# Kernel tuning notes

Hardware: AMD Instinct MI355X
Metric: run time of the kernel (lower is better)

Reference implementation:

```python
import jax, jax.numpy as jnp
import numpy as np

EMB = 1024
HEADS = 16
HEAD_DIM = EMB // HEADS
EPS = 1e-5


def setup_inputs() -> dict:
    key = jax.random.key(0)
    ks = jax.random.split(key, 10)
    B, T, D = 2, 2048, EMB
    s = 1.0 / np.sqrt(D)
    inp = {
        "x": jax.random.normal(ks[0], (B, T, D), dtype=jnp.float32),
        "wq": jax.random.normal(ks[1], (D, D), dtype=jnp.float32) * s,
        "bq": jnp.zeros((D,), jnp.float32),
        "wk": jax.random.normal(ks[2], (D, D), dtype=jnp.float32) * s,
        "bk": jnp.zeros((D,), jnp.float32),
        "wv": jax.random.normal(ks[3], (D, D), dtype=jnp.float32) * s,
        "bv": jnp.zeros((D,), jnp.float32),
        "wo": jax.random.normal(ks[4], (D, D), dtype=jnp.float32) * s,
        "bo": jnp.zeros((D,), jnp.float32),
        "gamma": jnp.ones((D,), jnp.float32),
        "beta": jnp.zeros((D,), jnp.float32),
    }
    return inp


def _attention(x, wq, bq, wk, bk, wv, bv, wo, bo, gamma, beta):
    B, T, D = x.shape
    H, Hd = HEADS, HEAD_DIM
    q = (x @ wq + bq).reshape(B, T, H, Hd)
    k = (x @ wk + bk).reshape(B, T, H, Hd)
    v = (x @ wv + bv).reshape(B, T, H, Hd)
    # scores: [B, H, T, T]
    scores = jnp.einsum("bthd,bshd->bhts", q, k) / np.sqrt(Hd)
    attn = jax.nn.softmax(scores, axis=-1)  # dropout is identity in eval
    ctx = jnp.einsum("bhts,bshd->bthd", attn, v).reshape(B, T, D)
    out = ctx @ wo + bo
    y = x + out  # residual (dropout identity)
    mu = jnp.mean(y, axis=-1, keepdims=True)
    var = jnp.var(y, axis=-1, keepdims=True)
    return (y - mu) * jax.lax.rsqrt(var + EPS) * gamma + beta


def reference(x, wq, bq, wk, bk, wv, bv, wo, bo, gamma, beta):
    return _attention(x, wq, bq, wk, bk, wv, bv, wo, bo, gamma, beta)
```

## Files before the change

### kernel.cpp

```cpp
#include <hip/hip_runtime.h>

#define BSZ   2
#define TSEQ  2048
#define DMOD  1024
#define NHEAD 16
#define HDIM  64
#define MROW  (BSZ*TSEQ)
#define LNEPS 1e-5f
#define QSCALE 0.18033688011f

typedef __bf16 bf16x8 __attribute__((ext_vector_type(8)));
typedef float  f32x4  __attribute__((ext_vector_type(4)));
typedef unsigned short us8 __attribute__((ext_vector_type(8)));
typedef unsigned short us4 __attribute__((ext_vector_type(4)));

__device__ __forceinline__ unsigned short f2bf(float f) {
    unsigned u = __float_as_uint(f);
    u += 0x7FFF + ((u >> 16) & 1);
    return (unsigned short)(u >> 16);
}
__device__ __forceinline__ float bf2f(unsigned short u) {
    return __uint_as_float((unsigned)u << 16);
}

__device__ __forceinline__ float fexp2(float x) {
#if __has_builtin(__builtin_amdgcn_exp2f)
    return __builtin_amdgcn_exp2f(x);
#else
    return __expf(x * 0.6931471805599453f);
#endif
}

__device__ __forceinline__ void gld_lds16(const void* g, void* l) {
    __builtin_amdgcn_global_load_lds(
        (const __attribute__((address_space(1))) unsigned int*)g,
        (__attribute__((address_space(3))) unsigned int*)l, 16, 0, 0);
}

__global__ __launch_bounds__(256) void prep_k(
    const float* __restrict__ x,
    const float* __restrict__ wq, const float* __restrict__ wk,
    const float* __restrict__ wv, const float* __restrict__ wo,
    unsigned short* __restrict__ Xb,
    unsigned short* __restrict__ WqkvT, unsigned short* __restrict__ WoT)
{
    const int tid = threadIdx.x;
    if (blockIdx.x < 2048) {
        const size_t i = ((size_t)blockIdx.x * 256 + tid) * 8;
        float4 a = *(const float4*)&x[i];
        float4 b = *(const float4*)&x[i + 4];
        union { unsigned short u[8]; uint4 v; } o;
        o.u[0]=f2bf(a.x); o.u[1]=f2bf(a.y); o.u[2]=f2bf(a.z); o.u[3]=f2bf(a.w);
        o.u[4]=f2bf(b.x); o.u[5]=f2bf(b.y); o.u[6]=f2bf(b.z); o.u[7]=f2bf(b.w);
        *(uint4*)&Xb[i] = o.v;
        return;
    }
    __shared__ float T[64][68];
    const int id = blockIdx.x - 2048;
    const int z  = id >> 8;
    const int bx = id & 15;
    const int by = (id >> 4) & 15;
    const float* W = (z == 0) ? wq : (z == 1) ? wk : (z == 2) ? wv : wo;
    unsigned short* Wt = (z < 3) ? (WqkvT + (size_t)z*1024*1024) : WoT;
    const int lr = tid >> 4, lc = (tid & 15) * 4;
    #pragma unroll
    for (int p = 0; p < 4; ++p) {
        const int kk = p*16 + lr;
        float4 v = *(const float4*)&W[(size_t)(by*64 + kk)*1024 + bx*64 + lc];
        T[lc+0][kk] = v.x; T[lc+1][kk] = v.y; T[lc+2][kk] = v.z; T[lc+3][kk] = v.w;
    }
    __syncthreads();
    #pragma unroll
    for (int p = 0; p < 2; ++p) {
        const int nl = p*32 + (tid >> 3);
        const int kb = (tid & 7) * 8;
        float4 a = *(const float4*)&T[nl][kb];
        float4 b = *(const float4*)&T[nl][kb+4];
        union { unsigned short u[8]; uint4 v; } o;
        o.u[0]=f2bf(a.x); o.u[1]=f2bf(a.y); o.u[2]=f2bf(a.z); o.u[3]=f2bf(a.w);
        o.u[4]=f2bf(b.x); o.u[5]=f2bf(b.y); o.u[6]=f2bf(b.z); o.u[7]=f2bf(b.w);
        *(uint4*)&Wt[(size_t)(bx*64 + nl)*1024 + by*64 + kb] = o.v;
    }
}


#define PH_SYNC() do { __builtin_amdgcn_s_barrier(); \
    asm volatile("s_waitcnt lgkmcnt(0)" ::: "memory"); \
    __builtin_amdgcn_sched_barrier(0); } while (0)

template<int N>
__device__ __forceinline__ void vmwait() {
    if constexpr (N == 0)      asm volatile("s_waitcnt vmcnt(0)" ::: "memory");
    else if constexpr (N == 3) asm volatile("s_waitcnt vmcnt(3)" ::: "memory");
    else                       asm volatile("s_waitcnt vmcnt(4)" ::: "memory");
}

template<int NB>
struct CoreT {
    const unsigned short *sA, *sB;
    unsigned short *A0w, *A1w, *B0w, *B1w;
    const unsigned short *fA0, *fA1, *fB0, *fB1;
    int swz0, swz1;
};

__device__ __forceinline__ void stageA4(const unsigned short* s, unsigned short* d) {
    #pragma unroll
    for (int u = 0; u < 4; ++u) gld_lds16(s + u*64*1024, d + u*4096);
}
template<int NB>
__device__ __forceinline__ void stageBall(const unsigned short* s, unsigned short* d) {
    #pragma unroll
    for (int u = 0; u < NB; ++u) gld_lds16(s + u*64*1024, d + u*4096);
}
__device__ __forceinline__ void stageB01(const unsigned short* s, unsigned short* d) {
    gld_lds16(s, d); gld_lds16(s + 64*1024, d + 4096);
}
template<int NB>
__device__ __forceinline__ void stageBrest(const unsigned short* s, unsigned short* d) {
    #pragma unroll
    for (int u = 2; u < NB; ++u) gld_lds16(s + u*64*1024, d + u*4096);
}

template<int NB>
__device__ __forceinline__ void core_setup(CoreT<NB>& C, unsigned short* LDS,
    const unsigned short* A, const unsigned short* Bt, int bm, int bn, int kbase)
{
    const int tid = threadIdx.x;
    const int w = tid >> 6, lane = tid & 63;
    const int quad = lane >> 4, l16 = lane & 15;
    const int wm = w >> 2, wn = w & 3;
    const int r_l = lane >> 3, c_l = lane & 7;
    C.sA = A  + (size_t)(bm + w*8 + r_l)*1024 + (c_l ^ r_l)*8 + kbase;
    C.sB = Bt + (size_t)(bn + w*8 + r_l)*1024 + (c_l ^ r_l)*8 + kbase;
    unsigned short* A0 = LDS;
    unsigned short* A1 = LDS + 16384;
    unsigned short* B0 = LDS + 32768;
    unsigned short* B1 = B0 + NB*4096;
    C.A0w = A0 + w*512; C.A1w = A1 + w*512;
    C.B0w = B0 + w*512; C.B1w = B1 + w*512;
    C.fA0 = A0 + (wm*128 + l16)*64; C.fA1 = A1 + (wm*128 + l16)*64;
    C.fB0 = B0 + (wn*NB*16 + l16)*64;  C.fB1 = B1 + (wn*NB*16 + l16)*64;
    C.swz0 = ( quad      ^ (l16 & 7)) * 8;
    C.swz1 = ((4 + quad) ^ (l16 & 7)) * 8;
}

template<int NB>
__device__ __forceinline__ void ld_b(const CoreT<NB>& C, bf16x8 (&bfr)[NB][2],
                                     const unsigned short* fB) {
    #pragma unroll
    for (int n = 0; n < NB; ++n) {
        bfr[n][0] = *(const bf16x8*)(fB + n*1024 + C.swz0);
        bfr[n][1] = *(const bf16x8*)(fB + n*1024 + C.swz1);
    }
}

template<int Q, int NB>
__device__ __forceinline__ void ld_a(const CoreT<NB>& C, bf16x8 (&af)[2][2],
                                     const unsigned short* fA) {
    #pragma unroll
    for (int dm = 0; dm < 2; ++dm) {
        af[dm][0] = *(const bf16x8*)(fA + (Q*2+dm)*1024 + C.swz0);
        af[dm][1] = *(const bf16x8*)(fA + (Q*2+dm)*1024 + C.swz1);
    }
}

template<int Q, int NB>
__device__ __forceinline__ void mma_q(f32x4 (&acc)[8][NB], bf16x8 (&af)[2][2],
                                      bf16x8 (&bfr)[NB][2]) {
    __builtin_amdgcn_s_setprio(1);
    #pragma unroll
    for (int dm = 0; dm < 2; ++dm)
        #pragma unroll
        for (int n = 0; n < NB; ++n) {
            f32x4 t = acc[Q*2+dm][n];
            t = __builtin_amdgcn_mfma_f32_16x16x32_bf16(af[dm][0], bfr[n][0], t, 0, 0, 0);
            t = __builtin_amdgcn_mfma_f32_16x16x32_bf16(af[dm][1], bfr[n][1], t, 0, 0, 0);
            acc[Q*2+dm][n] = t;
        }
    __builtin_amdgcn_s_setprio(0);
}

template<int NIT, int NB>
__device__ __forceinline__ void core_kloop(const CoreT<NB>& C, f32x4 (&acc)[8][NB])
{
    stageA4(C.sA, C.A0w);
    stageBall<NB>(C.sB,      C.B0w);
    stageBall<NB>(C.sB + 64, C.B1w);
    vmwait<NB>();
    __builtin_amdgcn_s_barrier();

    bf16x8 bfr[NB][2];
    bf16x8 af[2][2];

    #pragma unroll 1
    for (int it = 0; it < NIT - 1; ++it) {
        const int kk = it * 128;
        ld_b<NB>(C, bfr, C.fB0);
        ld_a<0,NB>(C, af, C.fA0);
        stageA4(C.sA + kk + 64, C.A1w);
        PH_SYNC();  mma_q<0,NB>(acc, af, bfr);
        __builtin_amdgcn_s_barrier();
        ld_a<1,NB>(C, af, C.fA0);
        stageB01(C.sB + kk + 128, C.B0w);
        PH_SYNC();  mma_q<1,NB>(acc, af, bfr);
        __builtin_amdgcn_s_barrier();
        ld_a<2,NB>(C, af, C.fA0);
        stageBrest<NB>(C.sB + kk + 128, C.B0w);
        PH_SYNC();  mma_q<2,NB>(acc, af, bfr);
        __builtin_amdgcn_s_barrier();
        ld_a<3,NB>(C, af, C.fA0);
        PH_SYNC();  mma_q<3,NB>(acc, af, bfr);
        vmwait<NB>();
        __builtin_amdgcn_s_barrier();
        ld_b<NB>(C, bfr, C.fB1);
        ld_a<0,NB>(C, af, C.fA1);
        stageA4(C.sA + kk + 128, C.A0w);
        PH_SYNC();  mma_q<0,NB>(acc, af, bfr);
        __builtin_amdgcn_s_barrier();
        ld_a<1,NB>(C, af, C.fA1);
        stageB01(C.sB + kk + 192, C.B1w);
        PH_SYNC();  mma_q<1,NB>(acc, af, bfr);
        __builtin_amdgcn_s_barrier();
        ld_a<2,NB>(C, af, C.fA1);
        stageBrest<NB>(C.sB + kk + 192, C.B1w);
        PH_SYNC();  mma_q<2,NB>(acc, af, bfr);
        __builtin_amdgcn_s_barrier();
        ld_a<3,NB>(C, af, C.fA1);
        PH_SYNC();  mma_q<3,NB>(acc, af, bfr);
        vmwait<NB>();
        __builtin_amdgcn_s_barrier();
    }

    {
        const int kk = (NIT - 1) * 128;
        ld_b<NB>(C, bfr, C.fB0);
        ld_a<0,NB>(C, af, C.fA0);
        stageA4(C.sA + kk + 64, C.A1w);
        PH_SYNC();  mma_q<0,NB>(acc, af, bfr);
        __builtin_amdgcn_s_barrier();
        ld_a<1,NB>(C, af, C.fA0); PH_SYNC(); mma_q<1,NB>(acc, af, bfr); __builtin_amdgcn_s_barrier();
        ld_a<2,NB>(C, af, C.fA0); PH_SYNC(); mma_q<2,NB>(acc, af, bfr); __builtin_amdgcn_s_barrier();
        ld_a<3,NB>(C, af, C.fA0); PH_SYNC(); mma_q<3,NB>(acc, af, bfr);
        vmwait<0>();
        __builtin_amdgcn_s_barrier();
        ld_b<NB>(C, bfr, C.fB1);
        ld_a<0,NB>(C, af, C.fA1); PH_SYNC(); mma_q<0,NB>(acc, af, bfr); __builtin_amdgcn_s_barrier();
        ld_a<1,NB>(C, af, C.fA1); PH_SYNC(); mma_q<1,NB>(acc, af, bfr); __builtin_amdgcn_s_barrier();
        ld_a<2,NB>(C, af, C.fA1); PH_SYNC(); mma_q<2,NB>(acc, af, bfr); __builtin_amdgcn_s_barrier();
        ld_a<3,NB>(C, af, C.fA1); PH_SYNC(); mma_q<3,NB>(acc, af, bfr);
    }
}

__global__ __launch_bounds__(512, 1) void gemm_qkv_k(
    const unsigned short* __restrict__ A, const unsigned short* __restrict__ Bt,
    const float* __restrict__ b0, const float* __restrict__ b1,
    const float* __restrict__ b2,
    unsigned short* __restrict__ oQ, unsigned short* __restrict__ oK,
    unsigned short* __restrict__ oV)
{
    extern __shared__ unsigned short LDS[];
    const int ob = blockIdx.x;
    const int wg = (ob & 7) * 32 + (ob >> 3);
    const int by = wg >> 4, bx = wg & 15;
    const int bm = by * 256, bn = bx * 192;

    CoreT<3> C;
    core_setup<3>(C, LDS, A, Bt, bm, bn, 0);

    f32x4 acc[8][3];
    #pragma unroll
    for (int i = 0; i < 8; ++i)
        #pragma unroll
        for (int j = 0; j < 3; ++j) acc[i][j] = (f32x4){0.f,0.f,0.f,0.f};

    core_kloop<8,3>(C, acc);

    const int tid = threadIdx.x;
    const int w = tid >> 6, lane = tid & 63;
    const int quad = lane >> 4, l16 = lane & 15;
    const int wm = w >> 2, wn = w & 3;
    #pragma unroll
    for (int n = 0; n < 3; ++n) {
        const int c0  = bn + wn*48 + n*16;
        const int seg = c0 >> 10;
        const int cl0 = c0 & 1023;
        if (seg < 2) {
            unsigned short* O = (seg == 0) ? oQ : oK;
            const float sc = (seg == 0) ? QSCALE : 1.0f;
            const float* bias = (seg == 0) ? b0 : b1;
            const int col = cl0 + l16;
            const float bs = bias[col];
            #pragma unroll
            for (int m = 0; m < 8; ++m)
                #pragma unroll
                for (int r = 0; r < 4; ++r) {
                    const int grow = bm + wm*128 + m*16 + quad*4 + r;
                    O[(size_t)grow*1024 + col] = f2bf((acc[m][n][r] + bs) * sc);
                }
        } else {
            const int ch = cl0 + l16;
            const float bs = b2[ch];
            #pragma unroll
            for (int m = 0; m < 8; ++m) {
                const int grow0 = bm + wm*128 + m*16 + quad*4;
                us4 o;
                #pragma unroll
                for (int r = 0; r < 4; ++r) o[r] = f2bf(acc[m][n][r] + bs);
                *(us4*)&oV[(size_t)ch*MROW + grow0] = o;
            }
        }
    }
}

__global__ __launch_bounds__(512, 2) void gemm_proj_k(
    const unsigned short* __restrict__ A, const unsigned short* __restrict__ Bt,
    unsigned short* __restrict__ P)
{
    extern __shared__ unsigned short LDS[];
    const int ob = blockIdx.x;
    const int wg = (ob & 7) * 8 + (ob >> 3);
    const int by = wg >> 2, bx = wg & 3;
    const int kz = blockIdx.y;
    const int bm = by * 256, bn = bx * 256;

    CoreT<4> C;
    core_setup<4>(C, LDS, A, Bt, bm, bn, kz * 256);

    f32x4 acc[8][4];
    #pragma unroll
    for (int i = 0; i < 8; ++i)
        #pragma unroll
        for (int j = 0; j < 4; ++j) acc[i][j] = (f32x4){0.f,0.f,0.f,0.f};

    core_kloop<2,4>(C, acc);

    const int tid = threadIdx.x;
    const int w = tid >> 6, lane = tid & 63;
    const int quad = lane >> 4, l16 = lane & 15;
    const int wm = w >> 2, wn = w & 3;
    unsigned short* O = P + (size_t)kz*MROW*1024;
    #pragma unroll
    for (int n = 0; n < 4; ++n) {
        const int col = bn + wn*64 + n*16 + l16;
        #pragma unroll
        for (int m = 0; m < 8; ++m)
            #pragma unroll
            for (int r = 0; r < 4; ++r) {
                const int grow = bm + wm*128 + m*16 + quad*4 + r;
                O[(size_t)grow*1024 + col] = f2bf(acc[m][n][r]);
            }
    }
}

__global__ __launch_bounds__(256, 2) void attn_k(
    const unsigned short* __restrict__ Qg,
    const unsigned short* __restrict__ Kg,
    const unsigned short* __restrict__ Vtg,
    unsigned short* __restrict__ CTX)
{
    extern __shared__ __align__(16) char lds_raw[];
    unsigned short* KV = (unsigned short*)lds_raw;
    unsigned short* Qs = (unsigned short*)lds_raw;
    float* Od = (float*)lds_raw;
    float* Ld = (float*)(lds_raw + 65536);

    const int tid  = threadIdx.x;
    const int wv   = tid >> 6;
    const int lane = tid & 63;
    const int quad = lane >> 4;
    const int l16  = lane & 15;
    const int wq   = wv & 1;
    const int wk   = wv >> 1;
    const int qb   = blockIdx.x * 128;
    const int h    = blockIdx.y;
    const int b    = blockIdx.z;

    {
        const int row = tid & 127, cb = (tid >> 7) * 32;
        const unsigned short* Qrow = Qg + ((size_t)(b*TSEQ + qb + row))*DMOD + h*HDIM + cb;
        #pragma unroll
        for (int j = 0; j < 4; ++j)
            *(us8*)&Qs[row*72 + cb + j*8] = *(const us8*)&Qrow[j*8];
    }
    __syncthreads();
    bf16x8 qf[4][2];
    #pragma unroll
    for (int nt = 0; nt < 4; ++nt)
        #pragma unroll
        for (int kh = 0; kh < 2; ++kh)
            qf[nt][kh] = *(const bf16x8*)&Qs[(wq*64 + nt*16 + l16)*72 + kh*32 + quad*8];
    __syncthreads();

    const int sr = lane >> 3;
    const int sc = lane & 7;
    const bool isK = (wv < 2);
    const int half = wv & 1;
    const unsigned short* gbase;
    unsigned int goff[8];
    unsigned short* ldstb;
    if (isK) {
        gbase = Kg + ((size_t)(b*TSEQ + half*1024))*DMOD + h*HDIM;
        #pragma unroll
        for (int s = 0; s < 8; ++s) {
            const int R = s*8 + sr;
            const int gc = sc ^ ((R ^ (R >> 2)) & 7);
            goff[s] = (unsigned)(R*DMOD + gc*8);
        }
        ldstb = KV + half*4096;
    } else {
        gbase = Vtg + ((size_t)(h*HDIM))*MROW + b*TSEQ + half*1024;
        #pragma unroll
        for (int s = 0; s < 8; ++s) {
            const int D = s*8 + sr;
            const int gc = sc ^ (D & 7);
            goff[s] = (unsigned)(D*MROW + gc*8);
        }
        ldstb = KV + 16384 + half*4096;
    }
    const size_t gstep = isK ? (size_t)64*DMOD : (size_t)64;

    const int rowA_l = (l16 >> 2)*8 + (l16 & 3);
    const int rowB_l = rowA_l + 4;
    const int swA = (rowA_l ^ (rowA_l >> 2)) & 7;
    const int swB = (rowB_l ^ (rowB_l >> 2)) & 7;

    bf16x8 onef;
    { union { unsigned short u[8]; bf16x8 v; } o1;
      #pragma unroll
      for (int i = 0; i < 8; ++i) o1.u[i] = 0x3F80;
      onef = o1.v; }

    f32x4 oacc[4][4];
    f32x4 lacc[4];
    #pragma unroll
    for (int dt = 0; dt < 4; ++dt)
        #pragma unroll
        for (int nt = 0; nt < 4; ++nt) oacc[dt][nt] = (f32x4){0.f,0.f,0.f,0.f};
    #pragma unroll
    for (int nt = 0; nt < 4; ++nt) lacc[nt] = (f32x4){0.f,0.f,0.f,0.f};

    #pragma unroll
    for (int s = 0; s < 8; ++s)
        gld_lds16(gbase + goff[s], ldstb + s*512);
    __syncthreads();

    for (int it = 0; it < 16; ++it) {
        const int cbuf = (it & 1) * 8192;
        if (it < 15) {
            const unsigned short* gn = gbase + (size_t)(it+1)*gstep;
            unsigned short* d = ldstb + (cbuf ^ 8192);
            #pragma unroll
            for (int s = 0; s < 8; ++s)
                gld_lds16(gn + goff[s], d + s*512);
        }
        __builtin_amdgcn_sched_barrier(0);
        const unsigned short* KsW = KV + cbuf + wk*4096;
        const unsigned short* VsW = KV + 16384 + cbuf + wk*4096;

        #pragma unroll
        for (int gl = 0; gl < 2; ++gl) {
            const int rA = gl*32 + rowA_l;
            const int rB = gl*32 + rowB_l;
            bf16x8 ka0 = *(const bf16x8*)&KsW[rA*64 + ((quad     ^ swA))*8];
            bf16x8 ka1 = *(const bf16x8*)&KsW[rA*64 + (((4+quad) ^ swA))*8];
            bf16x8 kb0 = *(const bf16x8*)&KsW[rB*64 + ((quad     ^ swB))*8];
            bf16x8 kb1 = *(const bf16x8*)&KsW[rB*64 + (((4+quad) ^ swB))*8];
            bf16x8 vf[4];
            #pragma unroll
            for (int dt = 0; dt < 4; ++dt)
                vf[dt] = *(const bf16x8*)&VsW[(dt*16 + l16)*64 + ((gl*4 + quad) ^ (l16 & 7))*8];

            f32x4 sA[4], sB[4];
            #pragma unroll
            for (int nt = 0; nt < 4; ++nt) {
                f32x4 z = (f32x4){0.f,0.f,0.f,0.f};
                z = __builtin_amdgcn_mfma_f32_16x16x32_bf16(ka0, qf[nt][0], z, 0, 0, 0);
                sA[nt] = __builtin_amdgcn_mfma_f32_16x16x32_bf16(ka1, qf[nt][1], z, 0, 0, 0);
                f32x4 z2 = (f32x4){0.f,0.f,0.f,0.f};
                z2 = __builtin_amdgcn_mfma_f32_16x16x32_bf16(kb0, qf[nt][0], z2, 0, 0, 0);
                sB[nt] = __builtin_amdgcn_mfma_f32_16x16x32_bf16(kb1, qf[nt][1], z2, 0, 0, 0);
            }
            bf16x8 pf[4];
            #pragma unroll
            for (int nt = 0; nt < 4; ++nt) {
                float eA[4], eB[4];
                #pragma unroll
                for (int r = 0; r < 4; ++r) { eA[r] = fexp2(sA[nt][r]); eB[r] = fexp2(sB[nt][r]); }
                union { unsigned d[4]; bf16x8 v; } up;
                up.d[0] = __builtin_amdgcn_perm(__float_as_uint(eA[1]), __float_as_uint(eA[0]), 0x07060302);
                up.d[1] = __builtin_amdgcn_perm(__float_as_uint(eA[3]), __float_as_uint(eA[2]), 0x07060302);
                up.d[2] = __builtin_amdgcn_perm(__float_as_uint(eB[1]), __float_as_uint(eB[0]), 0x07060302);
                up.d[3] = __builtin_amdgcn_perm(__float_as_uint(eB[3]), __float_as_uint(eB[2]), 0x07060302);
                pf[nt] = up.v;
            }
            __builtin_amdgcn_s_setprio(1);
            #pragma unroll
            for (int nt = 0; nt < 4; ++nt) {
                lacc[nt] = __builtin_amdgcn_mfma_f32_16x16x32_bf16(onef, pf[nt], lacc[nt], 0, 0, 0);
                #pragma unroll
                for (int dt = 0; dt < 4; ++dt)
                    oacc[dt][nt] = __builtin_amdgcn_mfma_f32_16x16x32_bf16(vf[dt], pf[nt], oacc[dt][nt], 0, 0, 0);
            }
            __builtin_amdgcn_s_setprio(0);
        }
        __syncthreads();
    }

    if (wk == 0) {
        float* od = Od + wq*64*68;
        #pragma unroll
        for (int nt = 0; nt < 4; ++nt) {
            #pragma unroll
            for (int dt = 0; dt < 4; ++dt)
                *(f32x4*)&od[(nt*16 + l16)*68 + dt*16 + quad*4] = oacc[dt][nt];
            if (quad == 0) Ld[wq*64 + nt*16 + l16] = lacc[nt][0];
        }
    }
    __syncthreads();
    if (wk == 1) {
        const float* od = Od + wq*64*68;
        #pragma unroll
        for (int nt = 0; nt < 4; ++nt) {
            const float l = Ld[wq*64 + nt*16 + l16] + lacc[nt][0];
            const float inv = 1.f / l;
            const int q = qb + wq*64 + nt*16 + l16;
            unsigned short* crow = CTX + ((size_t)(b*TSEQ + q))*DMOD + h*HDIM;
            #pragma unroll
            for (int dt = 0; dt < 4; ++dt) {
                f32x4 p = *(const f32x4*)&od[(nt*16 + l16)*68 + dt*16 + quad*4];
                us4 o;
                #pragma unroll
                for (int r = 0; r < 4; ++r) o[r] = f2bf((p[r] + oacc[dt][nt][r]) * inv);
                *(us4*)&crow[dt*16 + quad*4] = o;
            }
        }
    }
}

__global__ __launch_bounds__(256) void red_ln_k(
    const float* __restrict__ x, const unsigned short* __restrict__ P,
    const float* __restrict__ bo,
    const float* __restrict__ gamma, const float* __restrict__ beta,
    float* __restrict__ out)
{
    __shared__ float rs[4], rss[4];
    const int row = blockIdx.x;
    const int tid = threadIdx.x;
    const int c = tid * 4;
    const float4 xv = *(const float4*)&x[(size_t)row*DMOD + c];
    const us4 p0 = *(const us4*)&P[(size_t)row*DMOD + c];
    const us4 p1 = *(const us4*)&P[(size_t)(MROW + row)*DMOD + c];
    const us4 p2 = *(const us4*)&P[(size_t)(2*MROW + row)*DMOD + c];
    const us4 p3 = *(const us4*)&P[(size_t)(3*MROW + row)*DMOD + c];
    const float4 bv4 = *(const float4*)&bo[c];
    const float v0 = xv.x + bf2f(p0[0]) + bf2f(p1[0]) + bf2f(p2[0]) + bf2f(p3[0]) + bv4.x;
    const float v1 = xv.y + bf2f(p0[1]) + bf2f(p1[1]) + bf2f(p2[1]) + bf2f(p3[1]) + bv4.y;
    const float v2 = xv.z + bf2f(p0[2]) + bf2f(p1[2]) + bf2f(p2[2]) + bf2f(p3[2]) + bv4.z;
    const float v3 = xv.w + bf2f(p0[3]) + bf2f(p1[3]) + bf2f(p2[3]) + bf2f(p3[3]) + bv4.w;
    float s  = v0 + v1 + v2 + v3;
    float ss = v0*v0 + v1*v1 + v2*v2 + v3*v3;
    #pragma unroll
    for (int o = 32; o > 0; o >>= 1) {
        s  += __shfl_down(s,  o, 64);
        ss += __shfl_down(ss, o, 64);
    }
    if ((tid & 63) == 0) { rs[tid >> 6] = s; rss[tid >> 6] = ss; }
    __syncthreads();
    s  = rs[0] + rs[1] + rs[2] + rs[3];
    ss = rss[0] + rss[1] + rss[2] + rss[3];
    const float mean = s * (1.f/DMOD);
    const float var  = ss * (1.f/DMOD) - mean*mean;
    const float rstd = rsqrtf(var + LNEPS);
    const float4 gv = *(const float4*)&gamma[c];
    const float4 bv = *(const float4*)&beta[c];
    float4 o;
    o.x = (v0 - mean)*rstd*gv.x + bv.x;
    o.y = (v1 - mean)*rstd*gv.y + bv.y;
    o.z = (v2 - mean)*rstd*gv.z + bv.z;
    o.w = (v3 - mean)*rstd*gv.w + bv.w;
    *(float4*)&out[(size_t)row*DMOD + c] = o;
}

extern "C" void kernel_launch(void* const* d_in, const int* in_sizes, int n_in,
                              void* d_out, int out_size, void* d_ws, size_t ws_size,
                              hipStream_t stream) {
    const float* x     = (const float*)d_in[0];
    const float* wq    = (const float*)d_in[1];
    const float* bq    = (const float*)d_in[2];
    const float* wk    = (const float*)d_in[3];
    const float* bk    = (const float*)d_in[4];
    const float* wvp   = (const float*)d_in[5];
    const float* bvp   = (const float*)d_in[6];
    const float* wo    = (const float*)d_in[7];
    const float* bo    = (const float*)d_in[8];
    const float* gamma = (const float*)d_in[9];
    const float* beta  = (const float*)d_in[10];
    float* out = (float*)d_out;

    unsigned short* Xb    = (unsigned short*)d_ws;
    unsigned short* WqkvT = Xb    + (size_t)MROW*DMOD;
    unsigned short* WoT   = WqkvT + (size_t)3072*1024;
    unsigned short* Qb    = WoT   + (size_t)1024*1024;
    unsigned short* Kb    = Qb    + (size_t)MROW*DMOD;
    unsigned short* VtG   = Kb    + (size_t)MROW*DMOD;
    unsigned short* CTXb  = VtG   + (size_t)DMOD*MROW;
    unsigned short* Pp    = CTXb  + (size_t)MROW*DMOD;

    prep_k<<<3072, 256, 0, stream>>>(x, wq, wk, wvp, wo, Xb, WqkvT, WoT);

    gemm_qkv_k<<<dim3(256), 512, 114688, stream>>>(
        Xb, WqkvT, bq, bk, bvp, Qb, Kb, VtG);

    attn_k<<<dim3(TSEQ/128, NHEAD, BSZ), 256, 66048, stream>>>(Qb, Kb, VtG, CTXb);

    gemm_proj_k<<<dim3(64, 4), 512, 131072, stream>>>(CTXb, WoT, Pp);

    red_ln_k<<<MROW, 256, 0, stream>>>(x, Pp, bo, gamma, beta, out);
}
```

Measured before the change: 193.7 us.

## Retile QKV, projection and attention kernels for different grid shapes and occupancy

The QKV GEMM moves from 256x192 tiles over 256 blocks to 256x256 tiles over 192 blocks, so each tile sits entirely within one Q/K/V segment. The projection GEMM uses 256x128 tiles with a 2-way split-K instead of 4-way, which halves the partial-sum traffic the LayerNorm reduction reads. Attention switches to 64-query blocks with a small single-buffered K/V LDS tile, a flattened swizzled grid over head and batch, and launch bounds of 4 blocks per CU, trading software double-buffering for higher occupancy. The attention loop now synchronises twice per iteration with no prefetch overlap, so load latency may be exposed.

```diff
diff --git a/kernel.cpp b/kernel.cpp
--- a/kernel.cpp
+++ b/kernel.cpp
@@ -91,6 +91,7 @@
 template<int N>
 __device__ __forceinline__ void vmwait() {
     if constexpr (N == 0)      asm volatile("s_waitcnt vmcnt(0)" ::: "memory");
+    else if constexpr (N == 2) asm volatile("s_waitcnt vmcnt(2)" ::: "memory");
     else if constexpr (N == 3) asm volatile("s_waitcnt vmcnt(3)" ::: "memory");
     else                       asm volatile("s_waitcnt vmcnt(4)" ::: "memory");
 }
@@ -260,35 +261,34 @@
 {
     extern __shared__ unsigned short LDS[];
     const int ob = blockIdx.x;
-    const int wg = (ob & 7) * 32 + (ob >> 3);
-    const int by = wg >> 4, bx = wg & 15;
-    const int bm = by * 256, bn = bx * 192;
-
-    CoreT<3> C;
-    core_setup<3>(C, LDS, A, Bt, bm, bn, 0);
-
-    f32x4 acc[8][3];
+    const int wg = (ob & 7) * 24 + (ob >> 3);
+    const int by = wg / 12, bx = wg - by*12;
+    const int bm = by * 256, bn = bx * 256;
+
+    CoreT<4> C;
+    core_setup<4>(C, LDS, A, Bt, bm, bn, 0);
+
+    f32x4 acc[8][4];
     #pragma unroll
     for (int i = 0; i < 8; ++i)
         #pragma unroll
-        for (int j = 0; j < 3; ++j) acc[i][j] = (f32x4){0.f,0.f,0.f,0.f};
-
-    core_kloop<8,3>(C, acc);
+        for (int j = 0; j < 4; ++j) acc[i][j] = (f32x4){0.f,0.f,0.f,0.f};
+
+    core_kloop<8,4>(C, acc);
 
     const int tid = threadIdx.x;
     const int w = tid >> 6, lane = tid & 63;
     const int quad = lane >> 4, l16 = lane & 15;
     const int wm = w >> 2, wn = w & 3;
-    #pragma unroll
-    for (int n = 0; n < 3; ++n) {
-        const int c0  = bn + wn*48 + n*16;
-        const int seg = c0 >> 10;
-        const int cl0 = c0 & 1023;
-        if (seg < 2) {
-            unsigned short* O = (seg == 0) ? oQ : oK;
-            const float sc = (seg == 0) ? QSCALE : 1.0f;
-            const float* bias = (seg == 0) ? b0 : b1;
-            const int col = cl0 + l16;
+    const int seg = bn >> 10;
+    const int cb  = bn & 1023;
+    if (seg < 2) {
+        unsigned short* O = (seg == 0) ? oQ : oK;
+        const float sc = (seg == 0) ? QSCALE : 1.0f;
+        const float* bias = (seg == 0) ? b0 : b1;
+        #pragma unroll
+        for (int n = 0; n < 4; ++n) {
+            const int col = cb + wn*64 + n*16 + l16;
             const float bs = bias[col];
             #pragma unroll
             for (int m = 0; m < 8; ++m)
@@ -297,8 +297,11 @@
                     const int grow = bm + wm*128 + m*16 + quad*4 + r;
                     O[(size_t)grow*1024 + col] = f2bf((acc[m][n][r] + bs) * sc);
                 }
-        } else {
-            const int ch = cl0 + l16;
+        }
+    } else {
+        #pragma unroll
+        for (int n = 0; n < 4; ++n) {
+            const int ch = cb + wn*64 + n*16 + l16;
             const float bs = b2[ch];
             #pragma unroll
             for (int m = 0; m < 8; ++m) {
@@ -318,21 +321,21 @@
 {
     extern __shared__ unsigned short LDS[];
     const int ob = blockIdx.x;
-    const int wg = (ob & 7) * 8 + (ob >> 3);
-    const int by = wg >> 2, bx = wg & 3;
+    const int wg = (ob & 7) * 16 + (ob >> 3);
+    const int by = wg >> 3, bx = wg & 7;
     const int kz = blockIdx.y;
-    const int bm = by * 256, bn = bx * 256;
-
-    CoreT<4> C;
-    core_setup<4>(C, LDS, A, Bt, bm, bn, kz * 256);
-
-    f32x4 acc[8][4];
+    const int bm = by * 256, bn = bx * 128;
+
+    CoreT<2> C;
+    core_setup<2>(C, LDS, A, Bt, bm, bn, kz * 512);
+
+    f32x4 acc[8][2];
     #pragma unroll
     for (int i = 0; i < 8; ++i)
         #pragma unroll
-        for (int j = 0; j < 4; ++j) acc[i][j] = (f32x4){0.f,0.f,0.f,0.f};
-
-    core_kloop<2,4>(C, acc);
+        for (int j = 0; j < 2; ++j) acc[i][j] = (f32x4){0.f,0.f,0.f,0.f};
+
+    core_kloop<4,2>(C, acc);
 
     const int tid = threadIdx.x;
     const int w = tid >> 6, lane = tid & 63;
@@ -340,8 +343,8 @@
     const int wm = w >> 2, wn = w & 3;
     unsigned short* O = P + (size_t)kz*MROW*1024;
     #pragma unroll
-    for (int n = 0; n < 4; ++n) {
-        const int col = bn + wn*64 + n*16 + l16;
+    for (int n = 0; n < 2; ++n) {
+        const int col = bn + wn*32 + n*16 + l16;
         #pragma unroll
         for (int m = 0; m < 8; ++m)
             #pragma unroll
@@ -352,17 +355,18 @@
     }
 }
 
-__global__ __launch_bounds__(256, 2) void attn_k(
+__global__ __launch_bounds__(256, 4) void attn_k(
     const unsigned short* __restrict__ Qg,
     const unsigned short* __restrict__ Kg,
     const unsigned short* __restrict__ Vtg,
     unsigned short* __restrict__ CTX)
 {
     extern __shared__ __align__(16) char lds_raw[];
-    unsigned short* KV = (unsigned short*)lds_raw;
+    unsigned short* Ks = (unsigned short*)lds_raw;
+    unsigned short* Vs = (unsigned short*)(lds_raw + 8192);
     unsigned short* Qs = (unsigned short*)lds_raw;
     float* Od = (float*)lds_raw;
-    float* Ld = (float*)(lds_raw + 65536);
+    float* Ld = (float*)(lds_raw + 17408);
 
     const int tid  = threadIdx.x;
     const int wv   = tid >> 6;
@@ -371,58 +375,72 @@
     const int l16  = lane & 15;
     const int wq   = wv & 1;
     const int wk   = wv >> 1;
-    const int qb   = blockIdx.x * 128;
-    const int h    = blockIdx.y;
-    const int b    = blockIdx.z;
+
+    const int n    = blockIdx.x;
+    const int slot = n >> 3;
+    const int grp  = (n & 7) + 8 * (slot >> 5);
+    const int qx   = slot & 31;
+    const int h    = grp >> 1;
+    const int b    = grp & 1;
+    const int qb   = qx * 64;
 
     {
-        const int row = tid & 127, cb = (tid >> 7) * 32;
-        const unsigned short* Qrow = Qg + ((size_t)(b*TSEQ + qb + row))*DMOD + h*HDIM + cb;
-        #pragma unroll
-        for (int j = 0; j < 4; ++j)
-            *(us8*)&Qs[row*72 + cb + j*8] = *(const us8*)&Qrow[j*8];
+        const int r  = tid >> 2;
+        const int cb = (tid & 3) * 16;
+        const unsigned short* Qrow = Qg + ((size_t)(b*TSEQ + qb + r))*DMOD + h*HDIM + cb;
+        *(us8*)&Qs[r*72 + cb]     = *(const us8*)&Qrow[0];
+        *(us8*)&Qs[r*72 + cb + 8] = *(const us8*)&Qrow[8];
     }
     __syncthreads();
-    bf16x8 qf[4][2];
-    #pragma unroll
-    for (int nt = 0; nt < 4; ++nt)
+    bf16x8 qf[2][2];
+    #pragma unroll
+    for (int nt = 0; nt < 2; ++nt)
         #pragma unroll
         for (int kh = 0; kh < 2; ++kh)
-            qf[nt][kh] = *(const bf16x8*)&Qs[(wq*64 + nt*16 + l16)*72 + kh*32 + quad*8];
+            qf[nt][kh] = *(const bf16x8*)&Qs[(wq*32 + nt*16 + l16)*72 + kh*32 + quad*8];
     __syncthreads();
 
     const int sr = lane >> 3;
     const int sc = lane & 7;
     const bool isK = (wv < 2);
-    const int half = wv & 1;
+    const int part = wv & 1;
     const unsigned short* gbase;
-    unsigned int goff[8];
-    unsigned short* ldstb;
+    unsigned int goff[4];
+    unsigned short* ldst;
     if (isK) {
-        gbase = Kg + ((size_t)(b*TSEQ + half*1024))*DMOD + h*HDIM;
-        #pragma unroll
-        for (int s = 0; s < 8; ++s) {
-            const int R = s*8 + sr;
+        gbase = Kg + ((size_t)(b*TSEQ))*DMOD + h*HDIM;
+        #pragma unroll
+        for (int s = 0; s < 4; ++s) {
+            const int R = part*32 + s*8 + sr;
             const int gc = sc ^ ((R ^ (R >> 2)) & 7);
             goff[s] = (unsigned)(R*DMOD + gc*8);
         }
-        ldstb = KV + half*4096;
+        ldst = Ks + part*2048;
     } else {
-        gbase = Vtg + ((size_t)(h*HDIM))*MROW + b*TSEQ + half*1024;
-        #pragma unroll
-        for (int s = 0; s < 8; ++s) {
-            const int D = s*8 + sr;
+        gbase = Vtg + ((size_t)(h*HDIM))*MROW + b*TSEQ;
+        #pragma unroll
+        for (int s = 0; s < 4; ++s) {
+            const int D = part*32 + s*8 + sr;
             const int gc = sc ^ (D & 7);
             goff[s] = (unsigned)(D*MROW + gc*8);
         }
-        ldstb = KV + 16384 + half*4096;
+        ldst = Vs + part*2048;
     }
     const size_t gstep = isK ? (size_t)64*DMOD : (size_t)64;
 
     const int rowA_l = (l16 >> 2)*8 + (l16 & 3);
-    const int rowB_l = rowA_l + 4;
-    const int swA = (rowA_l ^ (rowA_l >> 2)) & 7;
-    const int swB = (rowB_l ^ (rowB_l >> 2)) & 7;
+    const int rA = wk*32 + rowA_l;
+    const int rB = rA + 4;
+    const int swA = ((rA ^ (rA >> 2)) & 7);
+    const int swB = ((rB ^ (rB >> 2)) & 7);
+    const unsigned short* kA0 = &Ks[rA*64 + ( quad      ^ swA)*8];
+    const unsigned short* kA1 = &Ks[rA*64 + ((4 + quad) ^ swA)*8];
+    const unsigned short* kB0 = &Ks[rB*64 + ( quad      ^ swB)*8];
+    const unsigned short* kB1 = &Ks[rB*64 + ((4 + quad) ^ swB)*8];
+    const unsigned short* vp[4];
+    #pragma unroll
+    for (int dt = 0; dt < 4; ++dt)
+        vp[dt] = &Vs[(dt*16 + l16)*64 + ((wk*4 + quad) ^ (l16 & 7))*8];
 
     bf16x8 onef;
     { union { unsigned short u[8]; bf16x8 v; } o1;
@@ -430,100 +448,80 @@
       for (int i = 0; i < 8; ++i) o1.u[i] = 0x3F80;
       onef = o1.v; }
 
-    f32x4 oacc[4][4];
-    f32x4 lacc[4];
+    f32x4 oacc[4][2];
+    f32x4 lacc[2];
     #pragma unroll
     for (int dt = 0; dt < 4; ++dt)
         #pragma unroll
-        for (int nt = 0; nt < 4; ++nt) oacc[dt][nt] = (f32x4){0.f,0.f,0.f,0.f};
-    #pragma unroll
-    for (int nt = 0; nt < 4; ++nt) lacc[nt] = (f32x4){0.f,0.f,0.f,0.f};
-
-    #pragma unroll
-    for (int s = 0; s < 8; ++s)
-        gld_lds16(gbase + goff[s], ldstb + s*512);
-    __syncthreads();
-
-    for (int it = 0; it < 16; ++it) {
-        const int cbuf = (it & 1) * 8192;
-        if (it < 15) {
-            const unsigned short* gn = gbase + (size_t)(it+1)*gstep;
-            unsigned short* d = ldstb + (cbuf ^ 8192);
+        for (int nt = 0; nt < 2; ++nt) oacc[dt][nt] = (f32x4){0.f,0.f,0.f,0.f};
+    lacc[0] = (f32x4){0.f,0.f,0.f,0.f};
+    lacc[1] = (f32x4){0.f,0.f,0.f,0.f};
+
+    #pragma unroll 1
+    for (int it = 0; it < 32; ++it) {
+        __syncthreads();
+        #pragma unroll
+        for (int s = 0; s < 4; ++s)
+            gld_lds16(gbase + (size_t)it*gstep + goff[s], ldst + s*512);
+        __syncthreads();
+
+        bf16x8 ka0 = *(const bf16x8*)kA0;
+        bf16x8 ka1 = *(const bf16x8*)kA1;
+        bf16x8 kb0 = *(const bf16x8*)kB0;
+        bf16x8 kb1 = *(const bf16x8*)kB1;
+        bf16x8 vf[4];
+        #pragma unroll
+        for (int dt = 0; dt < 4; ++dt) vf[dt] = *(const bf16x8*)vp[dt];
+
+        bf16x8 pf[2];
+        #pragma unroll
+        for (int nt = 0; nt < 2; ++nt) {
+            f32x4 z = (f32x4){0.f,0.f,0.f,0.f};
+            z = __builtin_amdgcn_mfma_f32_16x16x32_bf16(ka0, qf[nt][0], z, 0, 0, 0);
+            f32x4 sA = __builtin_amdgcn_mfma_f32_16x16x32_bf16(ka1, qf[nt][1], z, 0, 0, 0);
+            f32x4 z2 = (f32x4){0.f,0.f,0.f,0.f};
+            z2 = __builtin_amdgcn_mfma_f32_16x16x32_bf16(kb0, qf[nt][0], z2, 0, 0, 0);
+            f32x4 sB = __builtin_amdgcn_mfma_f32_16x16x32_bf16(kb1, qf[nt][1], z2, 0, 0, 0);
+            float eA[4], eB[4];
             #pragma unroll
-            for (int s = 0; s < 8; ++s)
-                gld_lds16(gn + goff[s], d + s*512);
-        }
-        __builtin_amdgcn_sched_barrier(0);
-        const unsigned short* KsW = KV + cbuf + wk*4096;
-        const unsigned short* VsW = KV + 16384 + cbuf + wk*4096;
-
-        #pragma unroll
-        for (int gl = 0; gl < 2; ++gl) {
-            const int rA = gl*32 + rowA_l;
-            const int rB = gl*32 + rowB_l;
-            bf16x8 ka0 = *(const bf16x8*)&KsW[rA*64 + ((quad     ^ swA))*8];
-            bf16x8 ka1 = *(const bf16x8*)&KsW[rA*64 + (((4+quad) ^ swA))*8];
-            bf16x8 kb0 = *(const bf16x8*)&KsW[rB*64 + ((quad     ^ swB))*8];
-            bf16x8 kb1 = *(const bf16x8*)&KsW[rB*64 + (((4+quad) ^ swB))*8];
-            bf16x8 vf[4];
+            for (int r = 0; r < 4; ++r) { eA[r] = fexp2(sA[r]); eB[r] = fexp2(sB[r]); }
+            union { unsigned d[4]; bf16x8 v; } up;
+            up.d[0] = __builtin_amdgcn_perm(__float_as_uint(eA[1]), __float_as_uint(eA[0]), 0x07060302);
+            up.d[1] = __builtin_amdgcn_perm(__float_as_uint(eA[3]), __float_as_uint(eA[2]), 0x07060302);
+            up.d[2] = __builtin_amdgcn_perm(__float_as_uint(eB[1]), __float_as_uint(eB[0]), 0x07060302);
+            up.d[3] = __builtin_amdgcn_perm(__float_as_uint(eB[3]), __float_as_uint(eB[2]), 0x07060302);
+            pf[nt] = up.v;
+        }
+        __builtin_amdgcn_s_setprio(1);
+        #pragma unroll
+        for (int nt = 0; nt < 2; ++nt) {
+            lacc[nt] = __builtin_amdgcn_mfma_f32_16x16x32_bf16(onef, pf[nt], lacc[nt], 0, 0, 0);
             #pragma unroll
             for (int dt = 0; dt < 4; ++dt)
-                vf[dt] = *(const bf16x8*)&VsW[(dt*16 + l16)*64 + ((gl*4 + quad) ^ (l16 & 7))*8];
-
-            f32x4 sA[4], sB[4];
-            #pragma unroll
-            for (int nt = 0; nt < 4; ++nt) {
-                f32x4 z = (f32x4){0.f,0.f,0.f,0.f};
-                z = __builtin_amdgcn_mfma_f32_16x16x32_bf16(ka0, qf[nt][0], z, 0, 0, 0);
-                sA[nt] = __builtin_amdgcn_mfma_f32_16x16x32_bf16(ka1, qf[nt][1], z, 0, 0, 0);
-                f32x4 z2 = (f32x4){0.f,0.f,0.f,0.f};
-                z2 = __builtin_amdgcn_mfma_f32_16x16x32_bf16(kb0, qf[nt][0], z2, 0, 0, 0);
-                sB[nt] = __builtin_amdgcn_mfma_f32_16x16x32_bf16(kb1, qf[nt][1], z2, 0, 0, 0);
-            }
-            bf16x8 pf[4];
-            #pragma unroll
-            for (int nt = 0; nt < 4; ++nt) {
-                float eA[4], eB[4];
-                #pragma unroll
-                for (int r = 0; r < 4; ++r) { eA[r] = fexp2(sA[nt][r]); eB[r] = fexp2(sB[nt][r]); }
-                union { unsigned d[4]; bf16x8 v; } up;
-                up.d[0] = __builtin_amdgcn_perm(__float_as_uint(eA[1]), __float_as_uint(eA[0]), 0x07060302);
-                up.d[1] = __builtin_amdgcn_perm(__float_as_uint(eA[3]), __float_as_uint(eA[2]), 0x07060302);
-                up.d[2] = __builtin_amdgcn_perm(__float_as_uint(eB[1]), __float_as_uint(eB[0]), 0x07060302);
-                up.d[3] = __builtin_amdgcn_perm(__float_as_uint(eB[3]), __float_as_uint(eB[2]), 0x07060302);
-                pf[nt] = up.v;
-            }
-            __builtin_amdgcn_s_setprio(1);
-            #pragma unroll
-            for (int nt = 0; nt < 4; ++nt) {
-                lacc[nt] = __builtin_amdgcn_mfma_f32_16x16x32_bf16(onef, pf[nt], lacc[nt], 0, 0, 0);
-                #pragma unroll
-                for (int dt = 0; dt < 4; ++dt)
-                    oacc[dt][nt] = __builtin_amdgcn_mfma_f32_16x16x32_bf16(vf[dt], pf[nt], oacc[dt][nt], 0, 0, 0);
-            }
-            __builtin_amdgcn_s_setprio(0);
-        }
-        __syncthreads();
-    }
-
+                oacc[dt][nt] = __builtin_amdgcn_mfma_f32_16x16x32_bf16(vf[dt], pf[nt], oacc[dt][nt], 0, 0, 0);
+        }
+        __builtin_amdgcn_s_setprio(0);
+    }
+
+    __syncthreads();
     if (wk == 0) {
-        float* od = Od + wq*64*68;
-        #pragma unroll
-        for (int nt = 0; nt < 4; ++nt) {
+        float* od = Od + wq*32*68;
+        #pragma unroll
+        for (int nt = 0; nt < 2; ++nt) {
             #pragma unroll
             for (int dt = 0; dt < 4; ++dt)
                 *(f32x4*)&od[(nt*16 + l16)*68 + dt*16 + quad*4] = oacc[dt][nt];
-            if (quad == 0) Ld[wq*64 + nt*16 + l16] = lacc[nt][0];
+            if (quad == 0) Ld[wq*32 + nt*16 + l16] = lacc[nt][0];
         }
     }
     __syncthreads();
     if (wk == 1) {
-        const float* od = Od + wq*64*68;
-        #pragma unroll
-        for (int nt = 0; nt < 4; ++nt) {
-            const float l = Ld[wq*64 + nt*16 + l16] + lacc[nt][0];
+        const float* od = Od + wq*32*68;
+        #pragma unroll
+        for (int nt = 0; nt < 2; ++nt) {
+            const float l = Ld[wq*32 + nt*16 + l16] + lacc[nt][0];
             const float inv = 1.f / l;
-            const int q = qb + wq*64 + nt*16 + l16;
+            const int q = qb + wq*32 + nt*16 + l16;
             unsigned short* crow = CTX + ((size_t)(b*TSEQ + q))*DMOD + h*HDIM;
             #pragma unroll
             for (int dt = 0; dt < 4; ++dt) {
@@ -550,13 +548,11 @@
     const float4 xv = *(const float4*)&x[(size_t)row*DMOD + c];
     const us4 p0 = *(const us4*)&P[(size_t)row*DMOD + c];
     const us4 p1 = *(const us4*)&P[(size_t)(MROW + row)*DMOD + c];
-    const us4 p2 = *(const us4*)&P[(size_t)(2*MROW + row)*DMOD + c];
-    const us4 p3 = *(const us4*)&P[(size_t)(3*MROW + row)*DMOD + c];
     const float4 bv4 = *(const float4*)&bo[c];
-    const float v0 = xv.x + bf2f(p0[0]) + bf2f(p1[0]) + bf2f(p2[0]) + bf2f(p3[0]) + bv4.x;
-    const float v1 = xv.y + bf2f(p0[1]) + bf2f(p1[1]) + bf2f(p2[1]) + bf2f(p3[1]) + bv4.y;
-    const float v2 = xv.z + bf2f(p0[2]) + bf2f(p1[2]) + bf2f(p2[2]) + bf2f(p3[2]) + bv4.z;
-    const float v3 = xv.w + bf2f(p0[3]) + bf2f(p1[3]) + bf2f(p2[3]) + bf2f(p3[3]) + bv4.w;
+    const float v0 = xv.x + bf2f(p0[0]) + bf2f(p1[0]) + bv4.x;
+    const float v1 = xv.y + bf2f(p0[1]) + bf2f(p1[1]) + bv4.y;
+    const float v2 = xv.z + bf2f(p0[2]) + bf2f(p1[2]) + bv4.z;
+    const float v3 = xv.w + bf2f(p0[3]) + bf2f(p1[3]) + bv4.w;
     float s  = v0 + v1 + v2 + v3;
     float ss = v0*v0 + v1*v1 + v2*v2 + v3*v3;
     #pragma unroll
@@ -608,12 +604,12 @@
 
     prep_k<<<3072, 256, 0, stream>>>(x, wq, wk, wvp, wo, Xb, WqkvT, WoT);
 
-    gemm_qkv_k<<<dim3(256), 512, 114688, stream>>>(
+    gemm_qkv_k<<<dim3(192), 512, 131072, stream>>>(
         Xb, WqkvT, bq, bk, bvp, Qb, Kb, VtG);
 
-    attn_k<<<dim3(TSEQ/128, NHEAD, BSZ), 256, 66048, stream>>>(Qb, Kb, VtG, CTXb);
-
-    gemm_proj_k<<<dim3(64, 4), 512, 131072, stream>>>(CTXb, WoT, Pp);
+    attn_k<<<dim3(1024), 256, 17664, stream>>>(Qb, Kb, VtG, CTXb);
+
+    gemm_proj_k<<<dim3(128, 2), 512, 98304, stream>>>(CTXb, WoT, Pp);
 
     red_ln_k<<<MROW, 256, 0, stream>>>(x, Pp, bo, gamma, beta, out);
 }
```

Result: no change. 191.4 us (-1.2%).
